# Kernel optimization log

Hardware: AMD Instinct MI355X
Metric: run time of the kernel (lower is better)

Reference implementation:

```python
import jax, jax.numpy as jnp
import numpy as np

EMBED_DIM = 1024
NUM_HEADS = 8
PROJ_DIM = EMBED_DIM // NUM_HEADS  # 128
SIGMA = 1.0        # attn_param
DISP = 1           # attn_displacement
BATCH = 8
SEQ_LEN = 2048
# per-head hard-coded attention positions (length == num_heads)
POSITIONS = ['center', 'left', 'right', 'first', 'last', 'center', 'left', 'right']


def _head_centers(L):
    """Center of the analytic Gaussian per head and per query position. [H, L]"""
    i = jnp.arange(L, dtype=jnp.float32)
    centers = []
    for pos in POSITIONS:
        if pos == 'center':
            c = i
        elif pos == 'left':
            c = i - DISP
        elif pos == 'right':
            c = i + DISP
        elif pos == 'first':
            c = jnp.zeros_like(i)
        else:  # 'last' (no padding: last valid index is L-1)
            c = jnp.full_like(i, L - 1)
        centers.append(c)
    return jnp.stack(centers)  # [H, L]


def setup_inputs() -> dict:
    key = jax.random.key(0)
    k1, k2, k3 = jax.random.split(key, 3)
    x = jax.random.normal(k1, (BATCH, SEQ_LEN, EMBED_DIM), dtype=jnp.float32)
    # xavier-ish scale for square weights
    s = (6.0 / (EMBED_DIM + EMBED_DIM)) ** 0.5
    W_in = jax.random.uniform(k2, (EMBED_DIM, EMBED_DIM), dtype=jnp.float32, minval=-s, maxval=s)
    W_out = jax.random.uniform(k3, (EMBED_DIM, EMBED_DIM), dtype=jnp.float32, minval=-s, maxval=s)
    return {"x": x, "W_in": W_in, "W_out": W_out}


def reference(x, W_in, W_out):
    B, L, E = x.shape
    H, P = NUM_HEADS, PROJ_DIM
    # value projection (F.linear with input_weights), split into heads
    v = (x @ W_in.T).reshape(B, L, H, P).transpose(0, 2, 1, 3)  # [B, H, L, P]
    # analytic per-head attention weights: Gaussian in key-position around center
    j = jnp.arange(L, dtype=jnp.float32)
    c = _head_centers(L)                                         # [H, Lq]
    logits = -((j[None, None, :] - c[:, :, None]) ** 2) / (2.0 * SIGMA ** 2)  # [H, Lq, Lk]
    w = jax.nn.softmax(logits, axis=-1)                          # [H, Lq, Lk]
    # weighted value aggregation (torch.bmm(attn_weights, values) per head)
    attended = jnp.einsum('hqk,bhkp->bhqp', w, v)                # [B, H, L, P]
    attended = attended.transpose(0, 2, 1, 3).reshape(B, L, E)
    # bias-free output projection
    return attended @ W_out.T
```

## Files before the change

kernel.cpp:

```cpp
#include <hip/hip_runtime.h>
#include <stdint.h>

typedef unsigned short u16;
typedef unsigned int   u32;

typedef float  f32x4  __attribute__((ext_vector_type(4)));
typedef __bf16 bf16x8 __attribute__((ext_vector_type(8)));

__device__ __forceinline__ u16 f2bf(float f) {
  union { float f; u32 u; } c; c.f = f;
  u32 u = c.u + 0x7fffu + ((c.u >> 16) & 1u);
  return (u16)(u >> 16);
}
__device__ __forceinline__ float bf2f(u16 h) {
  union { u32 u; float f; } c; c.u = ((u32)h) << 16;
  return c.f;
}
__device__ __forceinline__ void gll16(const void* g, void* l) {
  __builtin_amdgcn_global_load_lds(
      (const __attribute__((address_space(1))) void*)g,
      (__attribute__((address_space(3))) void*)l, 16, 0, 0);
}

__global__ __launch_bounds__(256)
void cvt_all(const float4* __restrict__ x,  uint2* __restrict__ xb,  int n4x,
             const float4* __restrict__ wi, uint2* __restrict__ wib,
             const float4* __restrict__ wo, uint2* __restrict__ wob, int n4w) {
  int i = blockIdx.x * 256 + threadIdx.x;
  const float4* s; uint2* d; int j;
  if (i < n4x)            { s = x;  d = xb;  j = i; }
  else if (i < n4x + n4w) { s = wi; d = wib; j = i - n4x; }
  else                    { s = wo; d = wob; j = i - n4x - n4w; }
  float4 v = s[j];
  uint2 o;
  o.x = (u32)f2bf(v.x) | ((u32)f2bf(v.y) << 16);
  o.y = (u32)f2bf(v.z) | ((u32)f2bf(v.w) << 16);
  d[j] = o;
}

template <bool OUT_BF16>
__global__ __launch_bounds__(256, 4)
void gemm_nt_bf16(const u16* __restrict__ A, const u16* __restrict__ B,
                  void* __restrict__ Cout, int M, int N, int K) {
  __shared__ u16 As[128 * 64];
  __shared__ u16 Bs[128 * 64];
  const int t    = threadIdx.x;
  const int lane = t & 63;
  const int ml   = lane & 15;
  const int q    = lane >> 4;
  const int wave = t >> 6;
  const int wm   = wave >> 1;
  const int wn   = wave & 1;

  const int flat    = blockIdx.y * 8 + blockIdx.x;
  const int xcd     = flat & 7;
  const int slot    = flat >> 3;
  const int per_xcd = gridDim.y >> 3;
  const int mt      = xcd * per_xcd + (slot >> 3);
  const int nt      = slot & 7;
  const int m0      = mt * 128;
  const int n0      = nt * 128;

  f32x4 acc[4][4] = {};

  const int sr = t >> 3;
  const int gk = (((t & 7) ^ (sr & 7)) * 8);
  const u16* Ag = A + (size_t)(m0 + sr) * K + gk;
  const u16* Bg = B + (size_t)(n0 + sr) * K + gk;
  const int wb = (t & 192) * 16;
  char* AsB = (char*)As;
  char* BsB = (char*)Bs;

  for (int k0 = 0; k0 < K; k0 += 64) {
#pragma unroll
    for (int j = 0; j < 4; ++j) {
      gll16(Ag + (size_t)(32 * j) * K + k0, AsB + j * 4096 + wb);
      gll16(Bg + (size_t)(32 * j) * K + k0, BsB + j * 4096 + wb);
    }
    __syncthreads();
#pragma unroll
    for (int s = 0; s < 2; ++s) {
      bf16x8 af[4], bfv[4];
#pragma unroll
      for (int i = 0; i < 4; ++i) {
        const int R = wm * 64 + i * 16 + ml;
        af[i] = *reinterpret_cast<const bf16x8*>(
            &As[R * 64 + (((s * 4 + q) ^ (R & 7)) * 8)]);
      }
#pragma unroll
      for (int i = 0; i < 4; ++i) {
        const int R = wn * 64 + i * 16 + ml;
        bfv[i] = *reinterpret_cast<const bf16x8*>(
            &Bs[R * 64 + (((s * 4 + q) ^ (R & 7)) * 8)]);
      }
#pragma unroll
      for (int i = 0; i < 4; ++i)
#pragma unroll
        for (int j = 0; j < 4; ++j)
          acc[i][j] = __builtin_amdgcn_mfma_f32_16x16x32_bf16(af[i], bfv[j], acc[i][j], 0, 0, 0);
    }
    __syncthreads();
  }

  const int rowb = m0 + wm * 64 + q * 4;
  const int colb = n0 + wn * 64 + ml;
#pragma unroll
  for (int i = 0; i < 4; ++i)
#pragma unroll
    for (int j = 0; j < 4; ++j)
#pragma unroll
      for (int r = 0; r < 4; ++r) {
        size_t idx = (size_t)(rowb + i * 16 + r) * N + (colb + j * 16);
        float val = acc[i][j][r];
        if (OUT_BF16) ((u16*)Cout)[idx] = f2bf(val);
        else          ((float*)Cout)[idx] = val;
      }
}

__global__ __launch_bounds__(256)
void gauss_conv(const u16* __restrict__ v, u16* __restrict__ att, int L) {
  constexpr float wt[13] = {
    1.5229979744712628e-08f, 3.7266531720786709e-06f, 3.3546262790251185e-04f,
    1.1108996538242306e-02f, 1.3533528323661270e-01f, 6.0653065971263342e-01f,
    1.0f,
    6.0653065971263342e-01f, 1.3533528323661270e-01f, 1.1108996538242306e-02f,
    3.3546262790251185e-04f, 3.7266531720786709e-06f, 1.5229979744712628e-08f
  };
  const int t  = threadIdx.x;
  const int fg = t & 15;
  const int li = t >> 4;
  const int l  = blockIdx.x * 16 + li;
  const int h  = blockIdx.y;
  const int b  = blockIdx.z;
  int c;
  switch (h) {
    case 0: case 5: c = l;     break;
    case 1: case 6: c = l - 1; break;
    case 2: case 7: c = l + 1; break;
    case 3:         c = 0;     break;
    default:        c = L - 1; break;
  }
  const int fbase = h * 128 + fg * 8;
  const u16* vb = v + (size_t)b * L * 1024 + fbase;

  float a[8] = {};
  float Z = 0.f;
#pragma unroll
  for (int d = -6; d <= 6; ++d) {
    int idx = c + d;
    bool ok = (idx >= 0) && (idx < L);
    int ic = idx < 0 ? 0 : (idx >= L ? L - 1 : idx);
    float w = ok ? wt[d + 6] : 0.f;
    Z += w;
    uint4 p = *reinterpret_cast<const uint4*>(vb + (size_t)ic * 1024);
    a[0] = fmaf(w, bf2f((u16)(p.x & 0xffffu)), a[0]);
    a[1] = fmaf(w, bf2f((u16)(p.x >> 16)),     a[1]);
    a[2] = fmaf(w, bf2f((u16)(p.y & 0xffffu)), a[2]);
    a[3] = fmaf(w, bf2f((u16)(p.y >> 16)),     a[3]);
    a[4] = fmaf(w, bf2f((u16)(p.z & 0xffffu)), a[4]);
    a[5] = fmaf(w, bf2f((u16)(p.z >> 16)),     a[5]);
    a[6] = fmaf(w, bf2f((u16)(p.w & 0xffffu)), a[6]);
    a[7] = fmaf(w, bf2f((u16)(p.w >> 16)),     a[7]);
  }
  float inv = 1.0f / Z;
  uint4 o;
  o.x = (u32)f2bf(a[0] * inv) | ((u32)f2bf(a[1] * inv) << 16);
  o.y = (u32)f2bf(a[2] * inv) | ((u32)f2bf(a[3] * inv) << 16);
  o.z = (u32)f2bf(a[4] * inv) | ((u32)f2bf(a[5] * inv) << 16);
  o.w = (u32)f2bf(a[6] * inv) | ((u32)f2bf(a[7] * inv) << 16);
  *reinterpret_cast<uint4*>(att + (size_t)(b * L + l) * 1024 + fbase) = o;
}

extern "C" void kernel_launch(void* const* d_in, const int* in_sizes, int n_in,
                              void* d_out, int out_size, void* d_ws, size_t ws_size,
                              hipStream_t stream) {
  const int Bb = 8, L = 2048, E = 1024;
  const int M = Bb * L, N = E, K = E;

  const float* x  = (const float*)d_in[0];
  const float* Wi = (const float*)d_in[1];
  const float* Wo = (const float*)d_in[2];
  float* out = (float*)d_out;

  size_t offV  = (size_t)M * E * 2;
  size_t offWi = offV + (size_t)M * E * 2;
  size_t offWo = offWi + (size_t)E * E * 2;
  size_t need  = offWo + (size_t)E * E * 2;
  if (ws_size < need) return;

  u16* xb  = (u16*)d_ws;
  u16* v   = (u16*)((char*)d_ws + offV);
  u16* wib = (u16*)((char*)d_ws + offWi);
  u16* wob = (u16*)((char*)d_ws + offWo);
  u16* att = xb;

  int n4x = M * E / 4, n4w = E * E / 4;
  int nblk = (n4x + 2 * n4w) / 256;
  cvt_all<<<nblk, 256, 0, stream>>>((const float4*)x, (uint2*)xb, n4x,
                                    (const float4*)Wi, (uint2*)wib,
                                    (const float4*)Wo, (uint2*)wob, n4w);

  dim3 gg(N / 128, M / 128);
  gemm_nt_bf16<true ><<<gg, 256, 0, stream>>>(xb,  wib, v,   M, N, K);
  gauss_conv<<<dim3(L / 16, 8, Bb), 256, 0, stream>>>(v, att, L);
  gemm_nt_bf16<false><<<gg, 256, 0, stream>>>(att, wob, out, M, N, K);
}
```

Baseline: 213.0 us.

## Replace 128x128 GEMM with 256x256 double-buffered, phase-interleaved MFMA kernel

Both bf16 GEMMs now use a 512-thread block computing a 256x256 output tile. The kernel double-buffers 128 KB of LDS, filled by direct global-to-LDS loads, and splits each K-step into four barrier-separated phases. Each phase issues the next tile's prefetch and then runs MFMAs at raised wave priority, with explicit vmcnt waits. The goal is more data reuse per tile and hiding of global load latency behind compute. The cost is one resident block per CU and a single wave of 256 blocks, which makes tail and occupancy effects more sensitive.

```diff
diff --git a/kernel.cpp b/kernel.cpp
--- a/kernel.cpp
+++ b/kernel.cpp
@@ -6,6 +6,8 @@
 
 typedef float  f32x4  __attribute__((ext_vector_type(4)));
 typedef __bf16 bf16x8 __attribute__((ext_vector_type(8)));
+
+template <int V> struct ic { static constexpr int value = V; };
 
 __device__ __forceinline__ u16 f2bf(float f) {
   union { float f; u32 u; } c; c.f = f;
@@ -39,79 +41,110 @@
 }
 
 template <bool OUT_BF16>
-__global__ __launch_bounds__(256, 4)
-void gemm_nt_bf16(const u16* __restrict__ A, const u16* __restrict__ B,
-                  void* __restrict__ Cout, int M, int N, int K) {
-  __shared__ u16 As[128 * 64];
-  __shared__ u16 Bs[128 * 64];
-  const int t    = threadIdx.x;
-  const int lane = t & 63;
+__global__ __launch_bounds__(512, 2)
+void gemm_nt_256(const u16* __restrict__ A, const u16* __restrict__ B,
+                 void* __restrict__ Cout, int M, int N, int K) {
+  __shared__ u16 Ls[65536];
+  const int tid  = threadIdx.x;
+  const int lane = tid & 63;
+  const int wave = tid >> 6;
+  const int wm   = wave >> 2;
+  const int wn   = wave & 3;
   const int ml   = lane & 15;
   const int q    = lane >> 4;
-  const int wave = t >> 6;
-  const int wm   = wave >> 1;
-  const int wn   = wave & 1;
-
-  const int flat    = blockIdx.y * 8 + blockIdx.x;
-  const int xcd     = flat & 7;
-  const int slot    = flat >> 3;
-  const int per_xcd = gridDim.y >> 3;
-  const int mt      = xcd * per_xcd + (slot >> 3);
-  const int nt      = slot & 7;
-  const int m0      = mt * 128;
-  const int n0      = nt * 128;
-
-  f32x4 acc[4][4] = {};
-
-  const int sr = t >> 3;
-  const int gk = (((t & 7) ^ (sr & 7)) * 8);
-  const u16* Ag = A + (size_t)(m0 + sr) * K + gk;
-  const u16* Bg = B + (size_t)(n0 + sr) * K + gk;
-  const int wb = (t & 192) * 16;
-  char* AsB = (char*)As;
-  char* BsB = (char*)Bs;
-
-  for (int k0 = 0; k0 < K; k0 += 64) {
-#pragma unroll
-    for (int j = 0; j < 4; ++j) {
-      gll16(Ag + (size_t)(32 * j) * K + k0, AsB + j * 4096 + wb);
-      gll16(Bg + (size_t)(32 * j) * K + k0, BsB + j * 4096 + wb);
+  const int pc   = q ^ ((ml >> 2) & 3);
+
+  const int flat = blockIdx.y * 4 + blockIdx.x;
+  const int xcd  = flat & 7;
+  const int slot = flat >> 3;
+  const int mt   = xcd * (gridDim.y >> 3) + (slot >> 2);
+  const int nt   = slot & 3;
+  const int m0   = mt * 256;
+  const int n0   = nt * 256;
+
+  const int g    = (tid & 3) ^ ((tid >> 4) & 3);
+  const int srow = tid >> 2;
+  const u16* Ag = A + (size_t)(m0 + srow) * K + g * 8;
+  const u16* Bg = B + (size_t)(n0 + srow) * K + g * 8;
+  char* LsB = (char*)Ls;
+  const int wb = wave * 1024;
+
+  auto stageA = [&](int bufsel, int s, int k0) {
+    char* lb = LsB + (size_t)(bufsel * 4 + s) * 16384 + wb;
+    gll16(Ag + k0 + s * 32, lb);
+    gll16(Ag + (size_t)128 * K + k0 + s * 32, lb + 8192);
+  };
+  auto stageB = [&](int bufsel, int s, int k0) {
+    char* lb = LsB + (size_t)(bufsel * 4 + 2 + s) * 16384 + wb;
+    gll16(Bg + k0 + s * 32, lb);
+    gll16(Bg + (size_t)128 * K + k0 + s * 32, lb + 8192);
+  };
+
+  f32x4  acc[8][4] = {};
+  bf16x8 bfv[2][4];
+  const int aoff = (wm * 128 + ml) * 32 + pc * 8;
+  const int boff = (wn * 64 + ml) * 32 + pc * 8;
+
+  auto phase = [&](auto MHc, auto Sc, auto RDBc, int buf) {
+    constexpr int MH = MHc.value;
+    constexpr int S  = Sc.value;
+    __builtin_amdgcn_s_barrier();
+    __builtin_amdgcn_sched_barrier(0);
+    const u16* Ab = Ls + (size_t)(buf * 4 + S) * 8192;
+    const u16* Bb = Ls + (size_t)(buf * 4 + 2 + S) * 8192;
+    bf16x8 a[4];
+#pragma unroll
+    for (int i = 0; i < 4; ++i)
+      a[i] = *reinterpret_cast<const bf16x8*>(&Ab[aoff + MH * 2048 + i * 512]);
+    if constexpr (RDBc.value != 0) {
+#pragma unroll
+      for (int j = 0; j < 4; ++j)
+        bfv[S][j] = *reinterpret_cast<const bf16x8*>(&Bb[boff + j * 512]);
     }
-    __syncthreads();
-#pragma unroll
-    for (int s = 0; s < 2; ++s) {
-      bf16x8 af[4], bfv[4];
-#pragma unroll
-      for (int i = 0; i < 4; ++i) {
-        const int R = wm * 64 + i * 16 + ml;
-        af[i] = *reinterpret_cast<const bf16x8*>(
-            &As[R * 64 + (((s * 4 + q) ^ (R & 7)) * 8)]);
-      }
-#pragma unroll
-      for (int i = 0; i < 4; ++i) {
-        const int R = wn * 64 + i * 16 + ml;
-        bfv[i] = *reinterpret_cast<const bf16x8*>(
-            &Bs[R * 64 + (((s * 4 + q) ^ (R & 7)) * 8)]);
-      }
-#pragma unroll
-      for (int i = 0; i < 4; ++i)
-#pragma unroll
-        for (int j = 0; j < 4; ++j)
-          acc[i][j] = __builtin_amdgcn_mfma_f32_16x16x32_bf16(af[i], bfv[j], acc[i][j], 0, 0, 0);
-    }
-    __syncthreads();
+    __builtin_amdgcn_s_setprio(1);
+#pragma unroll
+    for (int i = 0; i < 4; ++i)
+#pragma unroll
+      for (int j = 0; j < 4; ++j)
+        acc[MH * 4 + i][j] = __builtin_amdgcn_mfma_f32_16x16x32_bf16(
+            a[i], bfv[S][j], acc[MH * 4 + i][j], 0, 0, 0);
+    __builtin_amdgcn_s_setprio(0);
+  };
+
+  stageA(0, 0, 0); stageB(0, 0, 0); stageA(0, 1, 0); stageB(0, 1, 0);
+
+  const int NT = K >> 6;
+  int buf = 0;
+  for (int t = 0; t < NT - 1; ++t, buf ^= 1) {
+    const int kn = (t + 1) << 6;
+    stageA(buf ^ 1, 0, kn);
+    asm volatile("s_waitcnt vmcnt(6)" ::: "memory");
+    phase(ic<0>{}, ic<0>{}, ic<1>{}, buf);
+    stageB(buf ^ 1, 0, kn);
+    asm volatile("s_waitcnt vmcnt(4)" ::: "memory");
+    phase(ic<0>{}, ic<1>{}, ic<1>{}, buf);
+    stageA(buf ^ 1, 1, kn);
+    phase(ic<1>{}, ic<0>{}, ic<0>{}, buf);
+    stageB(buf ^ 1, 1, kn);
+    phase(ic<1>{}, ic<1>{}, ic<0>{}, buf);
   }
-
-  const int rowb = m0 + wm * 64 + q * 4;
+  asm volatile("s_waitcnt vmcnt(4)" ::: "memory");
+  phase(ic<0>{}, ic<0>{}, ic<1>{}, buf);
+  asm volatile("s_waitcnt vmcnt(0)" ::: "memory");
+  phase(ic<0>{}, ic<1>{}, ic<1>{}, buf);
+  phase(ic<1>{}, ic<0>{}, ic<0>{}, buf);
+  phase(ic<1>{}, ic<1>{}, ic<0>{}, buf);
+
+  const int rowb = m0 + wm * 128 + q * 4;
   const int colb = n0 + wn * 64 + ml;
 #pragma unroll
-  for (int i = 0; i < 4; ++i)
-#pragma unroll
-    for (int j = 0; j < 4; ++j)
+  for (int mf = 0; mf < 8; ++mf)
+#pragma unroll
+    for (int nf = 0; nf < 4; ++nf)
 #pragma unroll
       for (int r = 0; r < 4; ++r) {
-        size_t idx = (size_t)(rowb + i * 16 + r) * N + (colb + j * 16);
-        float val = acc[i][j][r];
+        size_t idx = (size_t)(rowb + mf * 16 + r) * N + (colb + nf * 16);
+        float val = acc[mf][nf][r];
         if (OUT_BF16) ((u16*)Cout)[idx] = f2bf(val);
         else          ((float*)Cout)[idx] = val;
       }
@@ -149,10 +182,10 @@
   for (int d = -6; d <= 6; ++d) {
     int idx = c + d;
     bool ok = (idx >= 0) && (idx < L);
-    int ic = idx < 0 ? 0 : (idx >= L ? L - 1 : idx);
+    int ic_ = idx < 0 ? 0 : (idx >= L ? L - 1 : idx);
     float w = ok ? wt[d + 6] : 0.f;
     Z += w;
-    uint4 p = *reinterpret_cast<const uint4*>(vb + (size_t)ic * 1024);
+    uint4 p = *reinterpret_cast<const uint4*>(vb + (size_t)ic_ * 1024);
     a[0] = fmaf(w, bf2f((u16)(p.x & 0xffffu)), a[0]);
     a[1] = fmaf(w, bf2f((u16)(p.x >> 16)),     a[1]);
     a[2] = fmaf(w, bf2f((u16)(p.y & 0xffffu)), a[2]);
@@ -200,8 +233,8 @@
                                     (const float4*)Wi, (uint2*)wib,
                                     (const float4*)Wo, (uint2*)wob, n4w);
 
-  dim3 gg(N / 128, M / 128);
-  gemm_nt_bf16<true ><<<gg, 256, 0, stream>>>(xb,  wib, v,   M, N, K);
+  dim3 gg(N / 256, M / 256);
+  gemm_nt_256<true ><<<gg, 512, 0, stream>>>(xb,  wib, v,   M, N, K);
   gauss_conv<<<dim3(L / 16, 8, Bb), 256, 0, stream>>>(v, att, L);
-  gemm_nt_bf16<false><<<gg, 256, 0, stream>>>(att, wob, out, M, N, K);
-}
+  gemm_nt_256<false><<<gg, 512, 0, stream>>>(att, wob, out, M, N, K);
+}
```

Result: no change. 210.7 us (-1.1%).

## Apply Gaussian smoothing to input before value projection, fuse into conversion

Applied to the files above, without the earlier changes.

Uses linearity to swap the order of the Gaussian sequence convolution and the input projection. A single prep kernel now smooths fp32 x along the sequence into a padded bf16 buffer of 2050 rows per batch, which also performs the cast. The first GEMM then gathers a per-head shifted row (based on the column tile's head) from that buffer. This removes the separate gauss_conv kernel and its read/write pass over the intermediate. In exchange the convolution reads fp32 data (13 taps per output) and the first GEMM's A loads become gathered rows.

```diff
diff --git a/kernel.cpp b/kernel.cpp
--- a/kernel.cpp
+++ b/kernel.cpp
@@ -23,22 +23,63 @@
 }
 
 __global__ __launch_bounds__(256)
-void cvt_all(const float4* __restrict__ x,  uint2* __restrict__ xb,  int n4x,
-             const float4* __restrict__ wi, uint2* __restrict__ wib,
-             const float4* __restrict__ wo, uint2* __restrict__ wob, int n4w) {
-  int i = blockIdx.x * 256 + threadIdx.x;
-  const float4* s; uint2* d; int j;
-  if (i < n4x)            { s = x;  d = xb;  j = i; }
-  else if (i < n4x + n4w) { s = wi; d = wib; j = i - n4x; }
-  else                    { s = wo; d = wob; j = i - n4x - n4w; }
-  float4 v = s[j];
-  uint2 o;
-  o.x = (u32)f2bf(v.x) | ((u32)f2bf(v.y) << 16);
-  o.y = (u32)f2bf(v.z) | ((u32)f2bf(v.w) << 16);
-  d[j] = o;
-}
-
-template <bool OUT_BF16>
+void prep(const float* __restrict__ x, u16* __restrict__ y,
+          const float4* __restrict__ wi, uint2* __restrict__ wib,
+          const float4* __restrict__ wo, uint2* __restrict__ wob,
+          int nconvb, int L) {
+  constexpr float wt[13] = {
+    1.5229979744712628e-08f, 3.7266531720786709e-06f, 3.3546262790251185e-04f,
+    1.1108996538242306e-02f, 1.3533528323661270e-01f, 6.0653065971263342e-01f,
+    1.0f,
+    6.0653065971263342e-01f, 1.3533528323661270e-01f, 1.1108996538242306e-02f,
+    3.3546262790251185e-04f, 3.7266531720786709e-06f, 1.5229979744712628e-08f
+  };
+  const int t = threadIdx.x;
+  if ((int)blockIdx.x >= nconvb) {
+    int wid = ((int)blockIdx.x - nconvb) * 256 + t;
+    const int n4w = 1024 * 1024 / 4;
+    const float4* s; uint2* d; int j;
+    if (wid < n4w) { s = wi; d = wib; j = wid; }
+    else           { s = wo; d = wob; j = wid - n4w; }
+    float4 v = s[j];
+    uint2 o;
+    o.x = (u32)f2bf(v.x) | ((u32)f2bf(v.y) << 16);
+    o.y = (u32)f2bf(v.z) | ((u32)f2bf(v.w) << 16);
+    d[j] = o;
+    return;
+  }
+  int id    = (int)blockIdx.x * 256 + t;
+  int fg    = id & 127;
+  int rowid = id >> 7;
+  int b     = rowid / 2050;
+  int lp    = rowid - b * 2050 - 1;
+  const float* xb = x + (size_t)b * L * 1024 + fg * 8;
+  float a[8] = {};
+  float Z = 0.f;
+#pragma unroll
+  for (int d = -6; d <= 6; ++d) {
+    int idx = lp + d;
+    bool ok = (idx >= 0) && (idx < L);
+    int ic  = idx < 0 ? 0 : (idx >= L ? L - 1 : idx);
+    float w = ok ? wt[d + 6] : 0.f;
+    Z += w;
+    const float4* p = reinterpret_cast<const float4*>(xb + (size_t)ic * 1024);
+    float4 p0 = p[0], p1 = p[1];
+    a[0] = fmaf(w, p0.x, a[0]); a[1] = fmaf(w, p0.y, a[1]);
+    a[2] = fmaf(w, p0.z, a[2]); a[3] = fmaf(w, p0.w, a[3]);
+    a[4] = fmaf(w, p1.x, a[4]); a[5] = fmaf(w, p1.y, a[5]);
+    a[6] = fmaf(w, p1.z, a[6]); a[7] = fmaf(w, p1.w, a[7]);
+  }
+  float inv = 1.0f / Z;
+  uint4 o;
+  o.x = (u32)f2bf(a[0] * inv) | ((u32)f2bf(a[1] * inv) << 16);
+  o.y = (u32)f2bf(a[2] * inv) | ((u32)f2bf(a[3] * inv) << 16);
+  o.z = (u32)f2bf(a[4] * inv) | ((u32)f2bf(a[5] * inv) << 16);
+  o.w = (u32)f2bf(a[6] * inv) | ((u32)f2bf(a[7] * inv) << 16);
+  *reinterpret_cast<uint4*>(y + (size_t)rowid * 1024 + fg * 8) = o;
+}
+
+template <int AMODE, bool OUT_BF16>
 __global__ __launch_bounds__(256, 4)
 void gemm_nt_bf16(const u16* __restrict__ A, const u16* __restrict__ B,
                   void* __restrict__ Cout, int M, int N, int K) {
@@ -65,7 +106,28 @@
 
   const int sr = t >> 3;
   const int gk = (((t & 7) ^ (sr & 7)) * 8);
-  const u16* Ag = A + (size_t)(m0 + sr) * K + gk;
+  const u16* Agj[4];
+#pragma unroll
+  for (int j = 0; j < 4; ++j) {
+    const int mr = m0 + sr + 32 * j;
+    size_t arow;
+    if (AMODE == 0) {
+      arow = (size_t)mr;
+    } else {
+      const int b = mr >> 11, l = mr & 2047;
+      const int h = n0 >> 7;
+      int sfl;
+      switch (h) {
+        case 0: case 5: sfl = l + 1; break;
+        case 1: case 6: sfl = l;     break;
+        case 2: case 7: sfl = l + 2; break;
+        case 3:         sfl = 1;     break;
+        default:        sfl = 2048;  break;
+      }
+      arow = (size_t)b * 2050 + sfl;
+    }
+    Agj[j] = A + arow * K + gk;
+  }
   const u16* Bg = B + (size_t)(n0 + sr) * K + gk;
   const int wb = (t & 192) * 16;
   char* AsB = (char*)As;
@@ -74,7 +136,7 @@
   for (int k0 = 0; k0 < K; k0 += 64) {
 #pragma unroll
     for (int j = 0; j < 4; ++j) {
-      gll16(Ag + (size_t)(32 * j) * K + k0, AsB + j * 4096 + wb);
+      gll16(Agj[j] + k0, AsB + j * 4096 + wb);
       gll16(Bg + (size_t)(32 * j) * K + k0, BsB + j * 4096 + wb);
     }
     __syncthreads();
@@ -117,60 +179,6 @@
       }
 }
 
-__global__ __launch_bounds__(256)
-void gauss_conv(const u16* __restrict__ v, u16* __restrict__ att, int L) {
-  constexpr float wt[13] = {
-    1.5229979744712628e-08f, 3.7266531720786709e-06f, 3.3546262790251185e-04f,
-    1.1108996538242306e-02f, 1.3533528323661270e-01f, 6.0653065971263342e-01f,
-    1.0f,
-    6.0653065971263342e-01f, 1.3533528323661270e-01f, 1.1108996538242306e-02f,
-    3.3546262790251185e-04f, 3.7266531720786709e-06f, 1.5229979744712628e-08f
-  };
-  const int t  = threadIdx.x;
-  const int fg = t & 15;
-  const int li = t >> 4;
-  const int l  = blockIdx.x * 16 + li;
-  const int h  = blockIdx.y;
-  const int b  = blockIdx.z;
-  int c;
-  switch (h) {
-    case 0: case 5: c = l;     break;
-    case 1: case 6: c = l - 1; break;
-    case 2: case 7: c = l + 1; break;
-    case 3:         c = 0;     break;
-    default:        c = L - 1; break;
-  }
-  const int fbase = h * 128 + fg * 8;
-  const u16* vb = v + (size_t)b * L * 1024 + fbase;
-
-  float a[8] = {};
-  float Z = 0.f;
-#pragma unroll
-  for (int d = -6; d <= 6; ++d) {
-    int idx = c + d;
-    bool ok = (idx >= 0) && (idx < L);
-    int ic = idx < 0 ? 0 : (idx >= L ? L - 1 : idx);
-    float w = ok ? wt[d + 6] : 0.f;
-    Z += w;
-    uint4 p = *reinterpret_cast<const uint4*>(vb + (size_t)ic * 1024);
-    a[0] = fmaf(w, bf2f((u16)(p.x & 0xffffu)), a[0]);
-    a[1] = fmaf(w, bf2f((u16)(p.x >> 16)),     a[1]);
-    a[2] = fmaf(w, bf2f((u16)(p.y & 0xffffu)), a[2]);
-    a[3] = fmaf(w, bf2f((u16)(p.y >> 16)),     a[3]);
-    a[4] = fmaf(w, bf2f((u16)(p.z & 0xffffu)), a[4]);
-    a[5] = fmaf(w, bf2f((u16)(p.z >> 16)),     a[5]);
-    a[6] = fmaf(w, bf2f((u16)(p.w & 0xffffu)), a[6]);
-    a[7] = fmaf(w, bf2f((u16)(p.w >> 16)),     a[7]);
-  }
-  float inv = 1.0f / Z;
-  uint4 o;
-  o.x = (u32)f2bf(a[0] * inv) | ((u32)f2bf(a[1] * inv) << 16);
-  o.y = (u32)f2bf(a[2] * inv) | ((u32)f2bf(a[3] * inv) << 16);
-  o.z = (u32)f2bf(a[4] * inv) | ((u32)f2bf(a[5] * inv) << 16);
-  o.w = (u32)f2bf(a[6] * inv) | ((u32)f2bf(a[7] * inv) << 16);
-  *reinterpret_cast<uint4*>(att + (size_t)(b * L + l) * 1024 + fbase) = o;
-}
-
 extern "C" void kernel_launch(void* const* d_in, const int* in_sizes, int n_in,
                               void* d_out, int out_size, void* d_ws, size_t ws_size,
                               hipStream_t stream) {
@@ -182,26 +190,23 @@
   const float* Wo = (const float*)d_in[2];
   float* out = (float*)d_out;
 
-  size_t offV  = (size_t)M * E * 2;
+  size_t offV  = (size_t)Bb * 2050 * E * 2;
   size_t offWi = offV + (size_t)M * E * 2;
   size_t offWo = offWi + (size_t)E * E * 2;
   size_t need  = offWo + (size_t)E * E * 2;
   if (ws_size < need) return;
 
-  u16* xb  = (u16*)d_ws;
+  u16* y   = (u16*)d_ws;
   u16* v   = (u16*)((char*)d_ws + offV);
   u16* wib = (u16*)((char*)d_ws + offWi);
   u16* wob = (u16*)((char*)d_ws + offWo);
-  u16* att = xb;
-
-  int n4x = M * E / 4, n4w = E * E / 4;
-  int nblk = (n4x + 2 * n4w) / 256;
-  cvt_all<<<nblk, 256, 0, stream>>>((const float4*)x, (uint2*)xb, n4x,
-                                    (const float4*)Wi, (uint2*)wib,
-                                    (const float4*)Wo, (uint2*)wob, n4w);
+
+  const int nconvb = Bb * 2050 * (E / 8) / 256;
+  const int nwb    = 2 * (E * E / 4) / 256;
+  prep<<<nconvb + nwb, 256, 0, stream>>>(x, y, (const float4*)Wi, (uint2*)wib,
+                                         (const float4*)Wo, (uint2*)wob, nconvb, L);
 
   dim3 gg(N / 128, M / 128);
-  gemm_nt_bf16<true ><<<gg, 256, 0, stream>>>(xb,  wib, v,   M, N, K);
-  gauss_conv<<<dim3(L / 16, 8, Bb), 256, 0, stream>>>(v, att, L);
-  gemm_nt_bf16<false><<<gg, 256, 0, stream>>>(att, wob, out, M, N, K);
-}
+  gemm_nt_bf16<1, true ><<<gg, 256, 0, stream>>>(y, wib, v,   M, N, K);
+  gemm_nt_bf16<0, false><<<gg, 256, 0, stream>>>(v, wob, out, M, N, K);
+}
```

Result: slower. 280.6 us (+31.8%).
